# Performance work log

Hardware: AMD Instinct MI355X
Metric: run time of the kernel (lower is better)

## Reference

```python
import jax, jax.numpy as jnp
import numpy as np

N_NODES = 50000


def gcn_norm(edge_index, edge_weight, n):
    """PyG GCNConv normalization: add self-loops (weight 1), sym-normalize."""
    src, dst = edge_index[0], edge_index[1]
    loop = jnp.arange(n, dtype=src.dtype)
    src = jnp.concatenate([src, loop])
    dst = jnp.concatenate([dst, loop])
    w = jnp.concatenate([edge_weight, jnp.ones((n,), dtype=edge_weight.dtype)])
    deg = jax.ops.segment_sum(w, dst, num_segments=n)  # in-degree w/ self-loops
    dis = jnp.where(deg > 0, jax.lax.rsqrt(deg), 0.0)  # deg^{-1/2}, inf -> 0
    norm = dis[src] * w * dis[dst]                      # [E+N]
    return src, dst, norm


def gcn_conv(x, src, dst, norm, W, b):
    h = x @ W                                            # [N, F_out]
    msg = norm[:, None] * h[src]                         # gather + scale
    out = jax.ops.segment_sum(msg, dst, num_segments=x.shape[0])  # scatter-add
    return out + b


def setup_inputs() -> dict:
    key = jax.random.key(0)
    ks = jax.random.split(key, 10)
    n, e = N_NODES, 800000
    in_dim, hidden, out_dim = 256, 128, 64
    x = jax.random.normal(ks[0], (n, in_dim), dtype=jnp.float32)
    edge_index = jax.random.randint(ks[1], (2, e), 0, n, dtype=jnp.int32)
    edge_weight = jax.random.uniform(ks[2], (e,), dtype=jnp.float32)
    def glorot(k, fi, fo):
        lim = float(np.sqrt(6.0 / (fi + fo)))
        return jax.random.uniform(k, (fi, fo), minval=-lim, maxval=lim, dtype=jnp.float32)
    return {
        "x": x, "edge_index": edge_index, "edge_weight": edge_weight,
        "W1": glorot(ks[3], in_dim, hidden), "b1": jnp.zeros((hidden,), jnp.float32),
        "W2": glorot(ks[4], hidden, hidden), "b2": jnp.zeros((hidden,), jnp.float32),
        "W3": glorot(ks[5], hidden, out_dim), "b3": jnp.zeros((out_dim,), jnp.float32),
    }


def reference(x, edge_index, edge_weight, W1, b1, W2, b2, W3, b3):
    n = x.shape[0]
    src, dst, norm = gcn_norm(edge_index, edge_weight, n)  # cached=True: shared
    h = jax.nn.relu(gcn_conv(x, src, dst, norm, W1, b1))   # dropout: eval mode no-op
    h = jax.nn.relu(gcn_conv(h, src, dst, norm, W2, b2))
    h = gcn_conv(h, src, dst, norm, W3, b3)
    return h
```

## Files before the change

### kernel.cpp

```cpp
#include <hip/hip_runtime.h>
#include <hip/hip_bf16.h>
#include <stdint.h>

#define NODES 50000
#define EDGES 800000
#define R_REP 8
#define SCAN_TB 256
#define SCAN_NB ((NODES + SCAN_TB - 1) / SCAN_TB)

typedef short bf16x8 __attribute__((ext_vector_type(8)));
typedef float f32x4 __attribute__((ext_vector_type(4)));

__device__ __forceinline__ unsigned short f2bf(float f) {
    union { float f; unsigned u; } v; v.f = f;
    unsigned r = v.u + 0x7fff + ((v.u >> 16) & 1);
    return (unsigned short)(r >> 16);
}
__device__ __forceinline__ float bf2f(unsigned short h) {
    union { float f; unsigned u; } v; v.u = ((unsigned)h) << 16;
    return v.f;
}
__device__ __forceinline__ float bflo(unsigned hv) {
    union { float f; unsigned u; } v; v.u = hv << 16;
    return v.f;
}
__device__ __forceinline__ float bfhi(unsigned hv) {
    union { float f; unsigned u; } v; v.u = hv & 0xffff0000u;
    return v.f;
}


__global__ void k_init(unsigned long long* packed) {
    int i = blockIdx.x * blockDim.x + threadIdx.x;
    if (i < NODES * R_REP) packed[i] = 0ull;
}

__global__ void k_deg(const int* __restrict__ dst, const float* __restrict__ w,
                      unsigned long long* __restrict__ packed, int* __restrict__ rank) {
    int e = blockIdx.x * blockDim.x + threadIdx.x;
    int r = blockIdx.x & (R_REP - 1);
    if (e < EDGES) {
        int d = dst[e];
        unsigned fx = __float2uint_rn(w[e] * 16777216.0f);
        unsigned long long add = (1ull << 40) | (unsigned long long)fx;
        unsigned long long old = atomicAdd(&packed[(size_t)r * NODES + d], add);
        rank[e] = (int)(old >> 40);
    }
}


__global__ void k_scan1(const unsigned long long* __restrict__ packed,
                        float* __restrict__ dis, int* __restrict__ repoff,
                        int* __restrict__ pre, int* __restrict__ bsum) {
    __shared__ int sm[SCAN_TB];
    int t = threadIdx.x;
    int i = blockIdx.x * SCAN_TB + t;
    int v = 0;
    if (i < NODES) {
        unsigned long long degfx = 0;
        int off = 0;
#pragma unroll
        for (int r = 0; r < R_REP; r++) {
            unsigned long long pk = packed[(size_t)r * NODES + i];
            repoff[(size_t)r * NODES + i] = off;
            off += (int)(pk >> 40);
            degfx += (pk & 0xFFFFFFFFFFull);
        }
        v = off;
        float deg = 1.0f + (float)degfx * (1.0f / 16777216.0f);
        dis[i] = rsqrtf(deg);
    }
    sm[t] = v;
    __syncthreads();
    for (int off = 1; off < SCAN_TB; off <<= 1) {
        int x = (t >= off) ? sm[t - off] : 0;
        __syncthreads();
        sm[t] += x;
        __syncthreads();
    }
    if (i < NODES) pre[i] = sm[t] - v;
    if (t == SCAN_TB - 1) bsum[blockIdx.x] = sm[t];
}

__global__ void k_scan2(const int* __restrict__ bsum, int* __restrict__ boff,
                        int* __restrict__ rowptr) {
    __shared__ int sm[256];
    int t = threadIdx.x;
    int v = (t < SCAN_NB) ? bsum[t] : 0;
    sm[t] = v;
    __syncthreads();
    for (int off = 1; off < 256; off <<= 1) {
        int x = (t >= off) ? sm[t - off] : 0;
        __syncthreads();
        sm[t] += x;
        __syncthreads();
    }
    if (t < SCAN_NB) boff[t] = sm[t] - v;
    if (t == 255) rowptr[NODES] = sm[255];
}

__global__ void k_scan3(const int* __restrict__ pre, const int* __restrict__ boff,
                        int* __restrict__ rowptr) {
    int b = blockIdx.x;
    int i = b * SCAN_TB + threadIdx.x;
    if (i < NODES) rowptr[i] = pre[i] + boff[b];
}

__global__ void k_scatter(const int* __restrict__ src, const int* __restrict__ dst,
                          const float* __restrict__ w, const float* __restrict__ dis,
                          const int* __restrict__ rowptr, const int* __restrict__ repoff,
                          const int* __restrict__ rank, int2* __restrict__ rec) {
    int e = blockIdx.x * blockDim.x + threadIdx.x;
    int r = blockIdx.x & (R_REP - 1);
    if (e < EDGES) {
        int s = src[e], d = dst[e];
        float nrm = dis[s] * w[e] * dis[d];
        int pos = rowptr[d] + repoff[(size_t)r * NODES + d] + rank[e];
        int2 rc; rc.x = s; rc.y = __float_as_int(nrm);
        rec[pos] = rc;
    }
}

__device__ __forceinline__ void wfrag_one(const float* __restrict__ W, unsigned short* Wf,
                                          int idx, int K, int Nn) {
    int NT = Nn >> 4;
    int lane = idx & 63;
    int f = idx >> 6;
    int nt = f % NT;
    int k0 = (f / NT) << 5;
    int n = (nt << 4) + (lane & 15);
    int kk = k0 + ((lane >> 4) << 3);
    unsigned short o[8];
#pragma unroll
    for (int j = 0; j < 8; j++) o[j] = f2bf(W[(kk + j) * Nn + n]);
    ((uint4*)Wf)[idx] = *(uint4*)o;
}

__global__ void k_wfrag_all(const float* __restrict__ W1, unsigned short* Wf1,
                            const float* __restrict__ W2, unsigned short* Wf2,
                            const float* __restrict__ W3, unsigned short* Wf3) {
    int idx = blockIdx.x * blockDim.x + threadIdx.x;
    if (idx < 4096) wfrag_one(W1, Wf1, idx, 256, 128);
    else if (idx < 6144) wfrag_one(W2, Wf2, idx - 4096, 128, 128);
    else if (idx < 7168) wfrag_one(W3, Wf3, idx - 6144, 128, 64);
}

template <int K, int Nn, bool A_F32>
__global__ void k_gemm(const void* __restrict__ A_, const uint4* __restrict__ Wf,
                       unsigned short* __restrict__ Hout) {
    constexpr int NT = Nn / 16;
    int lane = threadIdx.x & 63;
    int wave = threadIdx.x >> 6;
    int tile = blockIdx.x * 4 + wave;
    if (tile * 16 >= NODES) return;
    int row = tile * 16 + (lane & 15);
    int kbase = (lane >> 4) * 8;

    f32x4 acc[NT];
#pragma unroll
    for (int i = 0; i < NT; i++) acc[i] = (f32x4){0.f, 0.f, 0.f, 0.f};

    for (int k0 = 0; k0 < K; k0 += 32) {
        bf16x8 a;
        if (A_F32) {
            const float* A = (const float*)A_;
            const float4* p = (const float4*)&A[(size_t)row * K + k0 + kbase];
            float4 u0 = p[0], u1 = p[1];
            unsigned short t[8];
            t[0] = f2bf(u0.x); t[1] = f2bf(u0.y); t[2] = f2bf(u0.z); t[3] = f2bf(u0.w);
            t[4] = f2bf(u1.x); t[5] = f2bf(u1.y); t[6] = f2bf(u1.z); t[7] = f2bf(u1.w);
            a = *(bf16x8*)t;
        } else {
            const unsigned short* A = (const unsigned short*)A_;
            a = *(const bf16x8*)&A[(size_t)row * K + k0 + kbase];
        }
        int fbase = (k0 >> 5) * NT;
#pragma unroll
        for (int nt = 0; nt < NT; nt++) {
            uint4 braw = Wf[(fbase + nt) * 64 + lane];
            bf16x8 b = *(bf16x8*)&braw;
            acc[nt] = __builtin_amdgcn_mfma_f32_16x16x32_bf16(a, b, acc[nt], 0, 0, 0);
        }
    }
    int r0 = (lane >> 4) * 4;
    int col = lane & 15;
#pragma unroll
    for (int nt = 0; nt < NT; nt++) {
#pragma unroll
        for (int r = 0; r < 4; r++) {
            int m = tile * 16 + r0 + r;
            Hout[(size_t)m * Nn + nt * 16 + col] = f2bf(acc[nt][r]);
        }
    }
}

template <int F, bool RELU, bool OUT_F32>
__global__ void k_agg(const unsigned short* __restrict__ H, const int2* __restrict__ rec,
                      const int* __restrict__ rowptr, const float* __restrict__ dis,
                      const float* __restrict__ bias, void* __restrict__ out_) {
    constexpr int VPT = F / 64;
    int lane = threadIdx.x & 63;
    int wave = threadIdx.x >> 6;
    int node = blockIdx.x * 4 + wave;
    if (node >= NODES) return;

    const unsigned* H32 = (const unsigned*)H;

    float sn = dis[node]; sn = sn * sn;
    float acc0, acc1 = 0.f;
    if (VPT == 2) {
        unsigned hv = H32[(size_t)node * 64 + lane];
        acc0 = sn * bflo(hv);
        acc1 = sn * bfhi(hv);
    } else {
        acc0 = sn * bf2f(H[(size_t)node * F + lane]);
    }

    int beg = rowptr[node], end = rowptr[node + 1];
    for (int c = beg; c < end; c += 64) {
        int nrem = end - c; if (nrem > 64) nrem = 64;
        int2 r; r.x = 0; r.y = 0;
        if (lane < nrem) r = rec[c + lane];
        int nceil = (nrem + 7) & ~7;
        for (int j = 0; j < nceil; j += 8) {
            int ss[8]; float nn[8];
#pragma unroll
            for (int q = 0; q < 8; q++) {
                ss[q] = __shfl(r.x, j + q);
                nn[q] = __shfl(__int_as_float(r.y), j + q);
            }
            if (VPT == 2) {
                unsigned hh[8];
#pragma unroll
                for (int q = 0; q < 8; q++) hh[q] = H32[(size_t)ss[q] * 64 + lane];
#pragma unroll
                for (int q = 0; q < 8; q++) {
                    acc0 += nn[q] * bflo(hh[q]);
                    acc1 += nn[q] * bfhi(hh[q]);
                }
            } else {
                unsigned short hh[8];
#pragma unroll
                for (int q = 0; q < 8; q++) hh[q] = H[(size_t)ss[q] * F + lane];
#pragma unroll
                for (int q = 0; q < 8; q++) acc0 += nn[q] * bf2f(hh[q]);
            }
        }
    }

    if (OUT_F32) {
        float* out = (float*)out_;
        if (VPT == 2) {
            float x0 = acc0 + bias[lane * 2];
            float x1 = acc1 + bias[lane * 2 + 1];
            if (RELU) { x0 = fmaxf(x0, 0.f); x1 = fmaxf(x1, 0.f); }
            out[(size_t)node * F + lane * 2] = x0;
            out[(size_t)node * F + lane * 2 + 1] = x1;
        } else {
            float x0 = acc0 + bias[lane];
            if (RELU) x0 = fmaxf(x0, 0.f);
            out[(size_t)node * F + lane] = x0;
        }
    } else {
        unsigned short* out = (unsigned short*)out_;
        if (VPT == 2) {
            float x0 = acc0 + bias[lane * 2];
            float x1 = acc1 + bias[lane * 2 + 1];
            if (RELU) { x0 = fmaxf(x0, 0.f); x1 = fmaxf(x1, 0.f); }
            unsigned packed = (unsigned)f2bf(x0) | ((unsigned)f2bf(x1) << 16);
            *(unsigned*)&out[(size_t)node * F + lane * 2] = packed;
        } else {
            float x0 = acc0 + bias[lane];
            if (RELU) x0 = fmaxf(x0, 0.f);
            out[(size_t)node * F + lane] = f2bf(x0);
        }
    }
}


extern "C" void kernel_launch(void* const* d_in, const int* in_sizes, int n_in,
                              void* d_out, int out_size, void* d_ws, size_t ws_size,
                              hipStream_t stream) {
    const float* x  = (const float*)d_in[0];
    const int*   ei = (const int*)d_in[1];
    const float* w  = (const float*)d_in[2];
    const float* W1 = (const float*)d_in[3];
    const float* b1 = (const float*)d_in[4];
    const float* W2 = (const float*)d_in[5];
    const float* b2 = (const float*)d_in[6];
    const float* W3 = (const float*)d_in[7];
    const float* b3 = (const float*)d_in[8];
    const int* src = ei;
    const int* dst = ei + EDGES;

    char* p = (char*)d_ws;
    auto alloc = [&](size_t n) { char* r = p; p += (n + 511) & ~(size_t)511; return r; };
    unsigned long long* packed = (unsigned long long*)alloc((size_t)NODES * R_REP * 8);
    float*          dis    = (float*)alloc(NODES * 4);
    int*            rowptr = (int*)alloc((NODES + 1) * 4);
    int*            repoff = (int*)alloc((size_t)NODES * R_REP * 4);
    int*            rank   = (int*)alloc(EDGES * 4);
    int*            pre    = (int*)alloc(NODES * 4);
    int*            bsum   = (int*)alloc(SCAN_NB * 4);
    int*            boff   = (int*)alloc(SCAN_NB * 4);
    int2*           rec    = (int2*)alloc(EDGES * 8);
    unsigned short* h      = (unsigned short*)alloc((size_t)NODES * 128 * 2);
    unsigned short* xb     = (unsigned short*)alloc((size_t)NODES * 128 * 2);
    unsigned short* wf1    = (unsigned short*)alloc(256 * 128 * 2);
    unsigned short* wf2    = (unsigned short*)alloc(128 * 128 * 2);
    unsigned short* wf3    = (unsigned short*)alloc(128 * 64 * 2);

    const int TB = 256;
    int nb_initR = (NODES * R_REP + TB - 1) / TB;
    int nb_edges = (EDGES + TB - 1) / TB;

    hipLaunchKernelGGL(k_init, dim3(nb_initR), dim3(TB), 0, stream, packed);
    hipLaunchKernelGGL(k_deg, dim3(nb_edges), dim3(TB), 0, stream, dst, w, packed, rank);
    hipLaunchKernelGGL(k_scan1, dim3(SCAN_NB), dim3(SCAN_TB), 0, stream, packed, dis, repoff, pre, bsum);
    hipLaunchKernelGGL(k_scan2, dim3(1), dim3(256), 0, stream, bsum, boff, rowptr);
    hipLaunchKernelGGL(k_scan3, dim3(SCAN_NB), dim3(SCAN_TB), 0, stream, pre, boff, rowptr);
    hipLaunchKernelGGL(k_scatter, dim3(nb_edges), dim3(TB), 0, stream, src, dst, w, dis, rowptr, repoff, rank, rec);

    hipLaunchKernelGGL(k_wfrag_all, dim3((7168 + TB - 1) / TB), dim3(TB), 0, stream,
                       W1, wf1, W2, wf2, W3, wf3);

    int nb_gemm = (NODES / 16 + 3) / 4;
    int nb_agg  = (NODES + 3) / 4;

    hipLaunchKernelGGL((k_gemm<256, 128, true>), dim3(nb_gemm), dim3(TB), 0, stream, (const void*)x, (const uint4*)wf1, h);
    hipLaunchKernelGGL((k_agg<128, true, false>), dim3(nb_agg), dim3(TB), 0, stream, h, rec, rowptr, dis, b1, (void*)xb);

    hipLaunchKernelGGL((k_gemm<128, 128, false>), dim3(nb_gemm), dim3(TB), 0, stream, (const void*)xb, (const uint4*)wf2, h);
    hipLaunchKernelGGL((k_agg<128, true, false>), dim3(nb_agg), dim3(TB), 0, stream, h, rec, rowptr, dis, b2, (void*)xb);

    hipLaunchKernelGGL((k_gemm<128, 64, false>), dim3(nb_gemm), dim3(TB), 0, stream, (const void*)xb, (const uint4*)wf3, h);
    hipLaunchKernelGGL((k_agg<64, false, true>), dim3(nb_agg), dim3(TB), 0, stream, h, rec, rowptr, dis, b3, d_out);
}
```

Baseline: 292.4 us.

## Fuse setup kernels, fold scan3 into scatter, simplify aggregation edge loop

Merges the init and weight-fragment kernels into a single setup kernel. Folds the rowptr finalisation (scan3) into the scatter kernel, which now computes each position from pre plus boff directly. This removes two launches. The aggregation kernel now has every lane read the eight edge records straight from memory instead of loading a 64-edge chunk and broadcasting it with shuffles, uses 32-bit index arithmetic, and marks the node index wave-uniform with readfirstlane. The risk is redundant broadcast loads of rec in the aggregation loop. When a node has no edges the clamped index end-1 falls outside its range, but the loop body does not run in that case.

```diff
diff --git a/kernel.cpp b/kernel.cpp
--- a/kernel.cpp
+++ b/kernel.cpp
@@ -30,9 +30,31 @@
 }
 
 
-__global__ void k_init(unsigned long long* packed) {
-    int i = blockIdx.x * blockDim.x + threadIdx.x;
-    if (i < NODES * R_REP) packed[i] = 0ull;
+__device__ __forceinline__ void wfrag_one(const float* __restrict__ W, unsigned short* Wf,
+                                          int idx, int K, int Nn) {
+    int NT = Nn >> 4;
+    int lane = idx & 63;
+    int f = idx >> 6;
+    int nt = f % NT;
+    int k0 = (f / NT) << 5;
+    int n = (nt << 4) + (lane & 15);
+    int kk = k0 + ((lane >> 4) << 3);
+    unsigned short o[8];
+#pragma unroll
+    for (int j = 0; j < 8; j++) o[j] = f2bf(W[(kk + j) * Nn + n]);
+    ((uint4*)Wf)[idx] = *(uint4*)o;
+}
+
+__global__ void k_setup(unsigned long long* packed,
+                        const float* __restrict__ W1, unsigned short* Wf1,
+                        const float* __restrict__ W2, unsigned short* Wf2,
+                        const float* __restrict__ W3, unsigned short* Wf3) {
+    int idx = blockIdx.x * blockDim.x + threadIdx.x;
+    if (idx < NODES * R_REP) { packed[idx] = 0ull; return; }
+    int k = idx - NODES * R_REP;
+    if (k < 4096) wfrag_one(W1, Wf1, k, 256, 128);
+    else if (k < 6144) wfrag_one(W2, Wf2, k - 4096, 128, 128);
+    else if (k < 7168) wfrag_one(W3, Wf3, k - 6144, 128, 64);
 }
 
 __global__ void k_deg(const int* __restrict__ dst, const float* __restrict__ w,
@@ -99,50 +121,21 @@
     if (t == 255) rowptr[NODES] = sm[255];
 }
 
-__global__ void k_scan3(const int* __restrict__ pre, const int* __restrict__ boff,
-                        int* __restrict__ rowptr) {
-    int b = blockIdx.x;
-    int i = b * SCAN_TB + threadIdx.x;
-    if (i < NODES) rowptr[i] = pre[i] + boff[b];
-}
-
 __global__ void k_scatter(const int* __restrict__ src, const int* __restrict__ dst,
                           const float* __restrict__ w, const float* __restrict__ dis,
-                          const int* __restrict__ rowptr, const int* __restrict__ repoff,
-                          const int* __restrict__ rank, int2* __restrict__ rec) {
+                          const int* __restrict__ pre, const int* __restrict__ boff,
+                          const int* __restrict__ repoff, const int* __restrict__ rank,
+                          int2* __restrict__ rec, int* __restrict__ rowptr) {
     int e = blockIdx.x * blockDim.x + threadIdx.x;
     int r = blockIdx.x & (R_REP - 1);
+    if (e < NODES) rowptr[e] = pre[e] + boff[e >> 8];
     if (e < EDGES) {
         int s = src[e], d = dst[e];
         float nrm = dis[s] * w[e] * dis[d];
-        int pos = rowptr[d] + repoff[(size_t)r * NODES + d] + rank[e];
+        int pos = pre[d] + boff[d >> 8] + repoff[(size_t)r * NODES + d] + rank[e];
         int2 rc; rc.x = s; rc.y = __float_as_int(nrm);
         rec[pos] = rc;
     }
-}
-
-__device__ __forceinline__ void wfrag_one(const float* __restrict__ W, unsigned short* Wf,
-                                          int idx, int K, int Nn) {
-    int NT = Nn >> 4;
-    int lane = idx & 63;
-    int f = idx >> 6;
-    int nt = f % NT;
-    int k0 = (f / NT) << 5;
-    int n = (nt << 4) + (lane & 15);
-    int kk = k0 + ((lane >> 4) << 3);
-    unsigned short o[8];
-#pragma unroll
-    for (int j = 0; j < 8; j++) o[j] = f2bf(W[(kk + j) * Nn + n]);
-    ((uint4*)Wf)[idx] = *(uint4*)o;
-}
-
-__global__ void k_wfrag_all(const float* __restrict__ W1, unsigned short* Wf1,
-                            const float* __restrict__ W2, unsigned short* Wf2,
-                            const float* __restrict__ W3, unsigned short* Wf3) {
-    int idx = blockIdx.x * blockDim.x + threadIdx.x;
-    if (idx < 4096) wfrag_one(W1, Wf1, idx, 256, 128);
-    else if (idx < 6144) wfrag_one(W2, Wf2, idx - 4096, 128, 128);
-    else if (idx < 7168) wfrag_one(W3, Wf3, idx - 6144, 128, 64);
 }
 
 template <int K, int Nn, bool A_F32>
@@ -200,51 +193,48 @@
                       const float* __restrict__ bias, void* __restrict__ out_) {
     constexpr int VPT = F / 64;
     int lane = threadIdx.x & 63;
-    int wave = threadIdx.x >> 6;
-    int node = blockIdx.x * 4 + wave;
+    int node = blockIdx.x * 4 + (threadIdx.x >> 6);
     if (node >= NODES) return;
+    node = __builtin_amdgcn_readfirstlane(node);
 
     const unsigned* H32 = (const unsigned*)H;
 
     float sn = dis[node]; sn = sn * sn;
     float acc0, acc1 = 0.f;
     if (VPT == 2) {
-        unsigned hv = H32[(size_t)node * 64 + lane];
+        unsigned hv = H32[node * 64 + lane];
         acc0 = sn * bflo(hv);
         acc1 = sn * bfhi(hv);
     } else {
-        acc0 = sn * bf2f(H[(size_t)node * F + lane]);
+        acc0 = sn * bf2f(H[node * 64 + lane]);
     }
 
     int beg = rowptr[node], end = rowptr[node + 1];
-    for (int c = beg; c < end; c += 64) {
-        int nrem = end - c; if (nrem > 64) nrem = 64;
-        int2 r; r.x = 0; r.y = 0;
-        if (lane < nrem) r = rec[c + lane];
-        int nceil = (nrem + 7) & ~7;
-        for (int j = 0; j < nceil; j += 8) {
-            int ss[8]; float nn[8];
+    for (int j = beg; j < end; j += 8) {
+        int ss[8]; float nn[8];
+#pragma unroll
+        for (int q = 0; q < 8; q++) {
+            int idx = j + q;
+            idx = (idx < end - 1) ? idx : (end - 1);
+            int2 rc = rec[idx];
+            ss[q] = rc.x;
+            nn[q] = (j + q < end) ? __int_as_float(rc.y) : 0.0f;
+        }
+        if (VPT == 2) {
+            unsigned hh[8];
+#pragma unroll
+            for (int q = 0; q < 8; q++) hh[q] = H32[ss[q] * 64 + lane];
 #pragma unroll
             for (int q = 0; q < 8; q++) {
-                ss[q] = __shfl(r.x, j + q);
-                nn[q] = __shfl(__int_as_float(r.y), j + q);
+                acc0 += nn[q] * bflo(hh[q]);
+                acc1 += nn[q] * bfhi(hh[q]);
             }
-            if (VPT == 2) {
-                unsigned hh[8];
-#pragma unroll
-                for (int q = 0; q < 8; q++) hh[q] = H32[(size_t)ss[q] * 64 + lane];
-#pragma unroll
-                for (int q = 0; q < 8; q++) {
-                    acc0 += nn[q] * bflo(hh[q]);
-                    acc1 += nn[q] * bfhi(hh[q]);
-                }
-            } else {
-                unsigned short hh[8];
-#pragma unroll
-                for (int q = 0; q < 8; q++) hh[q] = H[(size_t)ss[q] * F + lane];
-#pragma unroll
-                for (int q = 0; q < 8; q++) acc0 += nn[q] * bf2f(hh[q]);
-            }
+        } else {
+            unsigned short hh[8];
+#pragma unroll
+            for (int q = 0; q < 8; q++) hh[q] = H[ss[q] * 64 + lane];
+#pragma unroll
+            for (int q = 0; q < 8; q++) acc0 += nn[q] * bf2f(hh[q]);
         }
     }
 
@@ -311,18 +301,15 @@
     unsigned short* wf3    = (unsigned short*)alloc(128 * 64 * 2);
 
     const int TB = 256;
-    int nb_initR = (NODES * R_REP + TB - 1) / TB;
+    int nb_setup = (NODES * R_REP + 7168 + TB - 1) / TB;
     int nb_edges = (EDGES + TB - 1) / TB;
 
-    hipLaunchKernelGGL(k_init, dim3(nb_initR), dim3(TB), 0, stream, packed);
+    hipLaunchKernelGGL(k_setup, dim3(nb_setup), dim3(TB), 0, stream, packed, W1, wf1, W2, wf2, W3, wf3);
     hipLaunchKernelGGL(k_deg, dim3(nb_edges), dim3(TB), 0, stream, dst, w, packed, rank);
     hipLaunchKernelGGL(k_scan1, dim3(SCAN_NB), dim3(SCAN_TB), 0, stream, packed, dis, repoff, pre, bsum);
     hipLaunchKernelGGL(k_scan2, dim3(1), dim3(256), 0, stream, bsum, boff, rowptr);
-    hipLaunchKernelGGL(k_scan3, dim3(SCAN_NB), dim3(SCAN_TB), 0, stream, pre, boff, rowptr);
-    hipLaunchKernelGGL(k_scatter, dim3(nb_edges), dim3(TB), 0, stream, src, dst, w, dis, rowptr, repoff, rank, rec);
-
-    hipLaunchKernelGGL(k_wfrag_all, dim3((7168 + TB - 1) / TB), dim3(TB), 0, stream,
-                       W1, wf1, W2, wf2, W3, wf3);
+    hipLaunchKernelGGL(k_scatter, dim3(nb_edges), dim3(TB), 0, stream, src, dst, w, dis,
+                       pre, boff, repoff, rank, rec, rowptr);
 
     int nb_gemm = (NODES / 16 + 3) / 4;
     int nb_agg  = (NODES + 3) / 4;
```

Measured after the change: 290.3 us. Within noise of the previous version (-0.7%).
